# Kernel optimization log

Hardware: AMD Instinct MI355X
Metric: run time of the kernel (lower is better)

Reference implementation:

```python
import jax, jax.numpy as jnp
import numpy as np

D_MODEL = 1024
N_HEADS = 16
D_K = D_MODEL // N_HEADS
D_FF = 4 * D_MODEL
LN_EPS = 1e-5


def _layer_norm(x, gamma, beta):
    mu = jnp.mean(x, axis=-1, keepdims=True)
    var = jnp.mean(jnp.square(x - mu), axis=-1, keepdims=True)
    return (x - mu) * jax.lax.rsqrt(var + LN_EPS) * gamma + beta


def setup_inputs() -> dict:
    key = jax.random.key(0)
    ks = jax.random.split(key, 16)
    s = 1.0 / np.sqrt(D_MODEL)
    sf = 1.0 / np.sqrt(D_FF)
    return {
        "x": jax.random.normal(ks[0], (4, 2048, D_MODEL), dtype=jnp.float32),
        "ln1_g": jnp.ones((D_MODEL,), jnp.float32),
        "ln1_b": jnp.zeros((D_MODEL,), jnp.float32),
        "ln2_g": jnp.ones((D_MODEL,), jnp.float32),
        "ln2_b": jnp.zeros((D_MODEL,), jnp.float32),
        "Wq": jax.random.uniform(ks[1], (D_MODEL, D_MODEL), jnp.float32, -s, s),
        "bq": jax.random.uniform(ks[2], (D_MODEL,), jnp.float32, -s, s),
        "Wk": jax.random.uniform(ks[3], (D_MODEL, D_MODEL), jnp.float32, -s, s),
        "bk": jax.random.uniform(ks[4], (D_MODEL,), jnp.float32, -s, s),
        "Wv": jax.random.uniform(ks[5], (D_MODEL, D_MODEL), jnp.float32, -s, s),
        "bv": jax.random.uniform(ks[6], (D_MODEL,), jnp.float32, -s, s),
        "Wo": jax.random.uniform(ks[7], (D_MODEL, D_MODEL), jnp.float32, -s, s),
        "bo": jax.random.uniform(ks[8], (D_MODEL,), jnp.float32, -s, s),
        "W1": jax.random.uniform(ks[9], (D_MODEL, D_FF), jnp.float32, -s, s),
        "b1": jax.random.uniform(ks[10], (D_FF,), jnp.float32, -s, s),
        "W2": jax.random.uniform(ks[11], (D_FF, D_MODEL), jnp.float32, -sf, sf),
        "b2": jax.random.uniform(ks[12], (D_MODEL,), jnp.float32, -sf, sf),
    }


def reference(x, ln1_g, ln1_b, ln2_g, ln2_b, Wq, bq, Wk, bk, Wv, bv, Wo, bo, W1, b1, W2, b2):
    B, S, _ = x.shape
    # --- pre-LN multi-head attention (dropout=0, mask=None) ---
    xn = _layer_norm(x, ln1_g, ln1_b)                      # [B,S,D]
    q = (xn @ Wq + bq).reshape(B, S, N_HEADS, D_K)          # [B,S,H,Dk]
    k = (xn @ Wk + bk).reshape(B, S, N_HEADS, D_K)
    v = (xn @ Wv + bv).reshape(B, S, N_HEADS, D_K)
    scores = jnp.einsum("bqhd,bkhd->bhqk", q, k) / np.sqrt(D_K)  # [B,H,S,S]
    attn = jax.nn.softmax(scores, axis=-1)
    ctx = jnp.einsum("bhqk,bkhd->bqhd", attn, v).reshape(B, S, D_MODEL)
    x = x + (ctx @ Wo + bo)
    # --- pre-LN FFN ---
    xn = _layer_norm(x, ln2_g, ln2_b)
    h = jax.nn.relu(xn @ W1 + b1)                           # [B,S,4D]
    x = x + (h @ W2 + b2)
    return x
```

## Files before the change

kernel.cpp:

```cpp
#include <hip/hip_runtime.h>
#include <cstdint>

typedef unsigned short u16;
typedef unsigned int u32;
typedef __bf16 bf16x8 __attribute__((ext_vector_type(8)));
typedef float f32x4 __attribute__((ext_vector_type(4)));
typedef u16 u16x8 __attribute__((ext_vector_type(8)));
typedef u32 u32x2 __attribute__((ext_vector_type(2)));

#define GLOBAL_AS __attribute__((address_space(1)))
#define LDS_AS __attribute__((address_space(3)))

__device__ __forceinline__ u16 f2b(float f) {
  u32 u = __builtin_bit_cast(u32, f);
  u += 0x7fffu + ((u >> 16) & 1u);
  return (u16)(u >> 16);
}

__global__ void transpose_cvt(const float* __restrict__ in, u16* __restrict__ out,
                              int K, int N) {
  __shared__ float tile[32][33];
  const int tx = threadIdx.x, ty = threadIdx.y;
  const int n0 = blockIdx.x * 32, k0 = blockIdx.y * 32;
#pragma unroll
  for (int i = 0; i < 4; i++)
    tile[ty + i * 8][tx] = in[(size_t)(k0 + ty + i * 8) * N + n0 + tx];
  __syncthreads();
#pragma unroll
  for (int i = 0; i < 4; i++)
    out[(size_t)(n0 + ty + i * 8) * K + k0 + tx] = f2b(tile[tx][ty + i * 8]);
}

__global__ __launch_bounds__(256) void ln_fwd(const float* __restrict__ x,
                                              const float* __restrict__ gamma,
                                              const float* __restrict__ beta,
                                              u16* __restrict__ out) {
  const int wid = threadIdx.x >> 6, lane = threadIdx.x & 63;
  const size_t row = (size_t)blockIdx.x * 4 + wid;
  const float* xr = x + row * 1024;
  float4 v[4];
  float s = 0.f, s2 = 0.f;
#pragma unroll
  for (int i = 0; i < 4; i++) {
    v[i] = *(const float4*)(xr + i * 256 + lane * 4);
    s += v[i].x + v[i].y + v[i].z + v[i].w;
    s2 += v[i].x * v[i].x + v[i].y * v[i].y + v[i].z * v[i].z + v[i].w * v[i].w;
  }
#pragma unroll
  for (int m = 1; m < 64; m <<= 1) {
    s += __shfl_xor(s, m);
    s2 += __shfl_xor(s2, m);
  }
  const float mu = s * (1.f / 1024.f);
  const float var = s2 * (1.f / 1024.f) - mu * mu;
  const float rs = rsqrtf(var + 1e-5f);
  u16* orow = out + row * 1024;
#pragma unroll
  for (int i = 0; i < 4; i++) {
    float4 gv = *(const float4*)(gamma + i * 256 + lane * 4);
    float4 bv = *(const float4*)(beta + i * 256 + lane * 4);
    float y0 = (v[i].x - mu) * rs * gv.x + bv.x;
    float y1 = (v[i].y - mu) * rs * gv.y + bv.y;
    float y2 = (v[i].z - mu) * rs * gv.z + bv.z;
    float y3 = (v[i].w - mu) * rs * gv.w + bv.w;
    uint2 pk;
    pk.x = (u32)f2b(y0) | ((u32)f2b(y1) << 16);
    pk.y = (u32)f2b(y2) | ((u32)f2b(y3) << 16);
    *(uint2*)(orow + i * 256 + lane * 4) = pk;
  }
}

template <int MODE>
__global__ __launch_bounds__(256) void gemm_bt(
    const u16* __restrict__ A, const u16* __restrict__ BT,
    const float* __restrict__ b0, const float* __restrict__ b1,
    const float* __restrict__ b2, const float* __restrict__ res,
    void* __restrict__ outp, int M, int N, int K) {
  __shared__ __align__(16) u16 Alds[128 * 64];
  __shared__ __align__(16) u16 Blds[128 * 64];
  const int tid = threadIdx.x;
  const int wid = tid >> 6, lane = tid & 63;
  const int wm = wid >> 1, wn = wid & 1;
  const int g = lane >> 4, l15 = lane & 15;
  const int bm = blockIdx.y * 128, bn = blockIdx.x * 128;

  f32x4 acc[4][4] = {};

  const int srow = wid * 32 + (lane >> 3);
  const int scol = (lane & 7) * 8;
  const u16* Ag = A + (size_t)(bm + srow) * K + scol;
  const u16* Bg = BT + (size_t)(bn + srow) * K + scol;

  for (int k0 = 0; k0 < K; k0 += 64) {
    __syncthreads();
#pragma unroll
    for (int i = 0; i < 4; i++)
      __builtin_amdgcn_global_load_lds(
          (const GLOBAL_AS u32*)(Ag + (size_t)(i * 8) * K + k0),
          (LDS_AS u32*)&Alds[(wid * 32 + i * 8) * 64], 16, 0, 0);
#pragma unroll
    for (int i = 0; i < 4; i++)
      __builtin_amdgcn_global_load_lds(
          (const GLOBAL_AS u32*)(Bg + (size_t)(i * 8) * K + k0),
          (LDS_AS u32*)&Blds[(wid * 32 + i * 8) * 64], 16, 0, 0);
    __syncthreads();
#pragma unroll
    for (int ks = 0; ks < 2; ks++) {
      bf16x8 af[4], bfr[4];
#pragma unroll
      for (int mt = 0; mt < 4; mt++)
        af[mt] = *(const bf16x8*)&Alds[(wm * 64 + mt * 16 + l15) * 64 + ks * 32 + g * 8];
#pragma unroll
      for (int nt = 0; nt < 4; nt++)
        bfr[nt] = *(const bf16x8*)&Blds[(wn * 64 + nt * 16 + l15) * 64 + ks * 32 + g * 8];
#pragma unroll
      for (int mt = 0; mt < 4; mt++)
#pragma unroll
        for (int nt = 0; nt < 4; nt++)
          acc[mt][nt] = __builtin_amdgcn_mfma_f32_16x16x32_bf16(
              af[mt], bfr[nt], acc[mt][nt], 0, 0, 0);
    }
  }

  const float* bias = b0;
  float scale = 1.f;
  if (MODE == 0) {
    bias = (bn < 1024) ? b0 : (bn < 2048 ? b1 : b2);
    if (bn < 1024) scale = 0.18033688011112042f;
  }
#pragma unroll
  for (int mt = 0; mt < 4; mt++) {
#pragma unroll
    for (int nt = 0; nt < 4; nt++) {
      const int orow = bm + wm * 64 + mt * 16 + g * 4;
      const int ocol = bn + wn * 64 + nt * 16 + l15;
      const float bv = bias[MODE == 0 ? (ocol & 1023) : ocol];
#pragma unroll
      for (int r = 0; r < 4; r++) {
        const float v = acc[mt][nt][r] + bv;
        const size_t oi = (size_t)(orow + r) * N + ocol;
        if (MODE == 0)
          ((u16*)outp)[oi] = f2b(v * scale);
        else if (MODE == 1)
          ((u16*)outp)[oi] = f2b(v > 0.f ? v : 0.f);
        else
          ((float*)outp)[oi] = v + res[oi];
      }
    }
  }
}

__global__ __launch_bounds__(256) void attn_fwd(const u16* __restrict__ QKV,
                                                u16* __restrict__ ctx) {
  __shared__ __align__(16) u16 Klds[2][64 * 64];
  __shared__ __align__(16) u16 Vlds[2][64 * 64];
  const int tid = threadIdx.x;
  const int wid = tid >> 6, lane = tid & 63;
  const int g = lane >> 4, l15 = lane & 15;
  const int qt = blockIdx.x, h = blockIdx.y, b = blockIdx.z;

  const u16* Qbase = QKV + (size_t)(b * 2048 + qt * 64 + wid * 16) * 3072 + h * 64;
  bf16x8 qf[2];
#pragma unroll
  for (int ks = 0; ks < 2; ks++)
    qf[ks] = *(const bf16x8*)(Qbase + (size_t)l15 * 3072 + ks * 32 + g * 8);

  const u16* Kg = QKV + (size_t)(b * 2048) * 3072 + 1024 + h * 64;
  const u16* Vg = QKV + (size_t)(b * 2048) * 3072 + 2048 + h * 64;

  int kvK[2], colK[2], kvV[2], d0V[2];
#pragma unroll
  for (int i = 0; i < 2; i++) {
    const int p = tid + 256 * i;
    kvK[i] = p >> 3;
    colK[i] = ((p & 7) ^ (kvK[i] & 7)) << 3;
    kvV[i] = ((p >> 5) << 2) | ((p >> 1) & 3);
    d0V[i] = (((p >> 3) & 3) << 4) | ((p & 1) << 3);
  }

#define STAGE(bufidx, tt)                                                          \
  do {                                                                             \
    const size_t roff = (size_t)(tt) * 64 * 3072;                                  \
    _Pragma("unroll") for (int i = 0; i < 2; i++) {                                \
      __builtin_amdgcn_global_load_lds(                                            \
          (const GLOBAL_AS u32*)(Kg + roff + (size_t)kvK[i] * 3072 + colK[i]),     \
          (LDS_AS u32*)&Klds[bufidx][(i * 256 + wid * 64) * 8], 16, 0, 0);         \
      __builtin_amdgcn_global_load_lds(                                            \
          (const GLOBAL_AS u32*)(Vg + roff + (size_t)kvV[i] * 3072 + d0V[i]),      \
          (LDS_AS u32*)&Vlds[bufidx][(i * 256 + wid * 64) * 8], 16, 0, 0);         \
    }                                                                              \
  } while (0)

#define TRISSUE(dst, dtc)                                                          \
  do {                                                                             \
    _Pragma("unroll") for (int nt = 0; nt < 4; nt++) {                             \
      const u32 a_ = vb + (u32)((((nt * 4 + g) * 4 + (dtc)) << 7) + (l15 << 1));   \
      asm volatile("ds_read_b64_tr_b16 %0, %1" : "=v"(dst[nt]) : "v"(a_)           \
                   : "memory");                                                    \
    }                                                                              \
  } while (0)

  float mrun = -3.0e38f, lrun = 0.f;
  f32x4 cacc[4] = {};

  STAGE(0, 0);
  int cur = 0;
  for (int t = 0; t < 32; t++) {
    __syncthreads();
    if (t < 31) STAGE(cur ^ 1, t + 1);

    const u16* Kc = &Klds[cur][0];
    f32x4 s4[4] = {};
#pragma unroll
    for (int nt = 0; nt < 4; nt++) {
      const int kv = nt * 16 + l15;
      const int sw = kv & 7;
#pragma unroll
      for (int ks = 0; ks < 2; ks++) {
        bf16x8 kf = *(const bf16x8*)&Kc[kv * 64 + (((ks * 4 + g) ^ sw) << 3)];
        s4[nt] = __builtin_amdgcn_mfma_f32_16x16x32_bf16(kf, qf[ks], s4[nt], 0, 0, 0);
      }
    }

    float pm = s4[0][0];
#pragma unroll
    for (int nt = 0; nt < 4; nt++)
#pragma unroll
      for (int r = 0; r < 4; r++) pm = fmaxf(pm, s4[nt][r]);
    pm = fmaxf(pm, __shfl_xor(pm, 16));
    pm = fmaxf(pm, __shfl_xor(pm, 32));
    const float mn = fmaxf(mrun, pm);
    const float alpha = exp2f(mrun - mn);
    mrun = mn;

    float psum = 0.f;
    u32 w[4][2];
#pragma unroll
    for (int nt = 0; nt < 4; nt++) {
      const float p0 = exp2f(s4[nt][0] - mn);
      const float p1 = exp2f(s4[nt][1] - mn);
      const float p2 = exp2f(s4[nt][2] - mn);
      const float p3 = exp2f(s4[nt][3] - mn);
      psum += (p0 + p1) + (p2 + p3);
      asm("v_cvt_pk_bf16_f32 %0, %1, %2" : "=v"(w[nt][0]) : "v"(p0), "v"(p1));
      asm("v_cvt_pk_bf16_f32 %0, %1, %2" : "=v"(w[nt][1]) : "v"(p2), "v"(p3));
    }
    psum += __shfl_xor(psum, 16);
    psum += __shfl_xor(psum, 32);
    lrun = lrun * alpha + psum;
#pragma unroll
    for (int dt = 0; dt < 4; dt++) cacc[dt] *= alpha;

    const u32 vb = (u32)(uintptr_t)(const LDS_AS u16*)&Vlds[cur][0];
    u32x2 vf[2][4];
    TRISSUE(vf[0], 0);
#pragma unroll
    for (int dt = 0; dt < 4; dt++) {
      if (dt < 3) TRISSUE(vf[(dt + 1) & 1], dt + 1);
      if (dt < 3)
        asm volatile("s_waitcnt lgkmcnt(4)" ::: "memory");
      else
        asm volatile("s_waitcnt lgkmcnt(0)" ::: "memory");
      __builtin_amdgcn_sched_barrier(0);
#pragma unroll
      for (int nt = 0; nt < 4; nt++) {
        const u32x2 pf = {w[nt][0], w[nt][1]};
        asm volatile("v_mfma_f32_16x16x16_bf16 %0, %1, %2, %0"
                     : "+v"(cacc[dt])
                     : "v"(vf[dt & 1][nt]), "v"(pf));
      }
    }
    cur ^= 1;
  }
#undef STAGE
#undef TRISSUE

  asm volatile("s_nop 7" :::);
  asm volatile("s_nop 7" :::);

  const float inv = 1.f / lrun;
  u16* op = ctx + (size_t)(b * 2048 + qt * 64 + wid * 16 + l15) * 1024 + h * 64 + g * 4;
#pragma unroll
  for (int dt = 0; dt < 4; dt++) {
    u32 lo, hi;
    const float c0 = cacc[dt][0] * inv, c1 = cacc[dt][1] * inv;
    const float c2 = cacc[dt][2] * inv, c3 = cacc[dt][3] * inv;
    asm("v_cvt_pk_bf16_f32 %0, %1, %2" : "=v"(lo) : "v"(c0), "v"(c1));
    asm("v_cvt_pk_bf16_f32 %0, %1, %2" : "=v"(hi) : "v"(c2), "v"(c3));
    *(u32x2*)(op + dt * 16) = (u32x2){lo, hi};
  }
}

extern "C" void kernel_launch(void* const* d_in, const int* in_sizes, int n_in,
                              void* d_out, int out_size, void* d_ws, size_t ws_size,
                              hipStream_t stream) {
  const float* x = (const float*)d_in[0];
  const float* ln1g = (const float*)d_in[1];
  const float* ln1b = (const float*)d_in[2];
  const float* ln2g = (const float*)d_in[3];
  const float* ln2b = (const float*)d_in[4];
  const float* Wq = (const float*)d_in[5];
  const float* bq = (const float*)d_in[6];
  const float* Wk = (const float*)d_in[7];
  const float* bk = (const float*)d_in[8];
  const float* Wv = (const float*)d_in[9];
  const float* bv = (const float*)d_in[10];
  const float* Wo = (const float*)d_in[11];
  const float* bo = (const float*)d_in[12];
  const float* W1 = (const float*)d_in[13];
  const float* b1 = (const float*)d_in[14];
  const float* W2 = (const float*)d_in[15];
  const float* b2 = (const float*)d_in[16];

  char* ws = (char*)d_ws;
  u16* WqkvT = (u16*)(ws + 0);
  u16* WoT = (u16*)(ws + 6291456);
  u16* W1T = (u16*)(ws + 8388608);
  u16* W2T = (u16*)(ws + 16777216);
  u16* xn = (u16*)(ws + 25165824);
  float* x2 = (float*)(ws + 41943040);
  u16* ctx = (u16*)(ws + 75497472);
  u16* big = (u16*)(ws + 92274688);
  u16* QKVb = big;
  u16* hbuf = big;
  float* outF = (float*)d_out;

  const dim3 tb(32, 8);
  transpose_cvt<<<dim3(32, 32), tb, 0, stream>>>(Wq, WqkvT, 1024, 1024);
  transpose_cvt<<<dim3(32, 32), tb, 0, stream>>>(Wk, WqkvT + 1024 * 1024, 1024, 1024);
  transpose_cvt<<<dim3(32, 32), tb, 0, stream>>>(Wv, WqkvT + 2048 * 1024, 1024, 1024);
  transpose_cvt<<<dim3(32, 32), tb, 0, stream>>>(Wo, WoT, 1024, 1024);
  transpose_cvt<<<dim3(128, 32), tb, 0, stream>>>(W1, W1T, 1024, 4096);
  transpose_cvt<<<dim3(32, 128), tb, 0, stream>>>(W2, W2T, 4096, 1024);

  ln_fwd<<<dim3(2048), dim3(256), 0, stream>>>(x, ln1g, ln1b, xn);
  gemm_bt<0><<<dim3(24, 64), dim3(256), 0, stream>>>(xn, WqkvT, bq, bk, bv, nullptr,
                                                     (void*)QKVb, 8192, 3072, 1024);
  attn_fwd<<<dim3(32, 16, 4), dim3(256), 0, stream>>>(QKVb, ctx);
  gemm_bt<2><<<dim3(8, 64), dim3(256), 0, stream>>>(ctx, WoT, bo, nullptr, nullptr, x,
                                                    (void*)x2, 8192, 1024, 1024);
  ln_fwd<<<dim3(2048), dim3(256), 0, stream>>>(x2, ln2g, ln2b, xn);
  gemm_bt<1><<<dim3(32, 64), dim3(256), 0, stream>>>(xn, W1T, b1, nullptr, nullptr,
                                                     nullptr, (void*)hbuf, 8192, 4096, 1024);
  gemm_bt<2><<<dim3(8, 64), dim3(256), 0, stream>>>(hbuf, W2T, b2, nullptr, nullptr, x2,
                                                    (void*)outF, 8192, 1024, 4096);
}
```

Measured before the change: 618.6 us.

## Replace GEMM with 8-wave double-buffered kernel using swizzled LDS and XCD tile remap

```diff
diff --git a/kernel.cpp b/kernel.cpp
--- a/kernel.cpp
+++ b/kernel.cpp
@@ -70,74 +70,122 @@
   }
 }
 
-template <int MODE>
-__global__ __launch_bounds__(256) void gemm_bt(
+template <int MF, int MODE>
+__global__ __launch_bounds__(512, 2) void gemm8p(
     const u16* __restrict__ A, const u16* __restrict__ BT,
     const float* __restrict__ b0, const float* __restrict__ b1,
     const float* __restrict__ b2, const float* __restrict__ res,
-    void* __restrict__ outp, int M, int N, int K) {
-  __shared__ __align__(16) u16 Alds[128 * 64];
-  __shared__ __align__(16) u16 Blds[128 * 64];
+    void* __restrict__ outp, int M, int N, int K, int gridN) {
+  constexpr int BM = MF * 32;
+  constexpr int AL = BM / 64;
+  __shared__ __align__(16) u16 Albuf[2][BM * 64];
+  __shared__ __align__(16) u16 Blbuf[2][256 * 64];
+
   const int tid = threadIdx.x;
-  const int wid = tid >> 6, lane = tid & 63;
-  const int wm = wid >> 1, wn = wid & 1;
+  const int lane = tid & 63, wid = tid >> 6;
+  const int wr = wid >> 2, wc = wid & 3;
   const int g = lane >> 4, l15 = lane & 15;
-  const int bm = blockIdx.y * 128, bn = blockIdx.x * 128;
-
-  f32x4 acc[4][4] = {};
-
-  const int srow = wid * 32 + (lane >> 3);
-  const int scol = (lane & 7) * 8;
-  const u16* Ag = A + (size_t)(bm + srow) * K + scol;
-  const u16* Bg = BT + (size_t)(bn + srow) * K + scol;
-
-  for (int k0 = 0; k0 < K; k0 += 64) {
-    __syncthreads();
-#pragma unroll
-    for (int i = 0; i < 4; i++)
-      __builtin_amdgcn_global_load_lds(
-          (const GLOBAL_AS u32*)(Ag + (size_t)(i * 8) * K + k0),
-          (LDS_AS u32*)&Alds[(wid * 32 + i * 8) * 64], 16, 0, 0);
-#pragma unroll
-    for (int i = 0; i < 4; i++)
-      __builtin_amdgcn_global_load_lds(
-          (const GLOBAL_AS u32*)(Bg + (size_t)(i * 8) * K + k0),
-          (LDS_AS u32*)&Blds[(wid * 32 + i * 8) * 64], 16, 0, 0);
-    __syncthreads();
-#pragma unroll
-    for (int ks = 0; ks < 2; ks++) {
-      bf16x8 af[4], bfr[4];
-#pragma unroll
-      for (int mt = 0; mt < 4; mt++)
-        af[mt] = *(const bf16x8*)&Alds[(wm * 64 + mt * 16 + l15) * 64 + ks * 32 + g * 8];
+  const int l8r = lane >> 3, l8c = lane & 7;
+
+  const int nwg = gridDim.x;
+  const int bid = blockIdx.x;
+  const int tile = (bid & 7) * (nwg >> 3) + (bid >> 3);
+  const int tm = tile / gridN, tn = tile - tm * gridN;
+  const int bm = tm * BM, bn = tn * 256;
+
+  const int scol = 8 * (l8c ^ l8r);
+  const u16* Ab = A + (size_t)(bm + wid * (AL * 8) + l8r) * K + scol;
+  const u16* Bb = BT + (size_t)(bn + wid * 32 + l8r) * K + scol;
+
+#define STAGE(bb, k0)                                                            \
+  do {                                                                           \
+    _Pragma("unroll") for (int i = 0; i < AL; i++)                               \
+        __builtin_amdgcn_global_load_lds(                                        \
+            (const GLOBAL_AS u32*)(Ab + (size_t)i * 8 * K + (k0)),               \
+            (LDS_AS u32*)&Albuf[bb][(wid * AL + i) * 512], 16, 0, 0);            \
+    _Pragma("unroll") for (int i = 0; i < 4; i++)                                \
+        __builtin_amdgcn_global_load_lds(                                        \
+            (const GLOBAL_AS u32*)(Bb + (size_t)i * 8 * K + (k0)),               \
+            (LDS_AS u32*)&Blbuf[bb][(wid * 4 + i) * 512], 16, 0, 0);             \
+  } while (0)
+
+#define VMCNT_STEADY()                                                           \
+  do {                                                                           \
+    if constexpr (MF == 8)                                                       \
+      asm volatile("s_waitcnt vmcnt(8)" ::: "memory");                           \
+    else                                                                         \
+      asm volatile("s_waitcnt vmcnt(6)" ::: "memory");                           \
+  } while (0)
+
+  f32x4 acc[MF][4] = {};
+  const int NT = K >> 6;
+
+  const int arow0 = (wr * (MF * 16) + l15) * 64;
+  const int brow0 = (wc * 64 + l15) * 64;
+  const int csw[2] = {8 * ((0 * 4 + g) ^ (l15 & 7)), 8 * ((1 * 4 + g) ^ (l15 & 7))};
+
+  STAGE(0, 0);
+  STAGE(1, 64);
+  VMCNT_STEADY();
+  __builtin_amdgcn_sched_barrier(0);
+  __builtin_amdgcn_s_barrier();
+
+  for (int t = 0; t < NT; t++) {
+    const int b = t & 1;
+    const u16* Alb = &Albuf[b][0];
+    const u16* Blb = &Blbuf[b][0];
+#pragma unroll
+    for (int q = 0; q < 4; q++) {
+      const int mh = q & 1, ks = q >> 1;
+      bf16x8 af[MF / 2], bf[4];
+#pragma unroll
+      for (int i = 0; i < MF / 2; i++)
+        af[i] = *(const bf16x8*)&Alb[arow0 + (mh * (MF / 2) + i) * (16 * 64) + csw[ks]];
 #pragma unroll
       for (int nt = 0; nt < 4; nt++)
-        bfr[nt] = *(const bf16x8*)&Blds[(wn * 64 + nt * 16 + l15) * 64 + ks * 32 + g * 8];
-#pragma unroll
-      for (int mt = 0; mt < 4; mt++)
+        bf[nt] = *(const bf16x8*)&Blb[brow0 + nt * (16 * 64) + csw[ks]];
+      __builtin_amdgcn_s_setprio(1);
+#pragma unroll
+      for (int i = 0; i < MF / 2; i++)
 #pragma unroll
         for (int nt = 0; nt < 4; nt++)
-          acc[mt][nt] = __builtin_amdgcn_mfma_f32_16x16x32_bf16(
-              af[mt], bfr[nt], acc[mt][nt], 0, 0, 0);
-    }
-  }
-
-  const float* bias = b0;
-  float scale = 1.f;
-  if (MODE == 0) {
-    bias = (bn < 1024) ? b0 : (bn < 2048 ? b1 : b2);
-    if (bn < 1024) scale = 0.18033688011112042f;
-  }
-#pragma unroll
-  for (int mt = 0; mt < 4; mt++) {
+          acc[mh * (MF / 2) + i][nt] = __builtin_amdgcn_mfma_f32_16x16x32_bf16(
+              af[i], bf[nt], acc[mh * (MF / 2) + i][nt], 0, 0, 0);
+      __builtin_amdgcn_s_setprio(0);
+    }
+    if (t + 1 < NT) {
+      __builtin_amdgcn_s_barrier();
+      if (t + 2 < NT) {
+        STAGE(b, (t + 2) * 64);
+        VMCNT_STEADY();
+      } else {
+        asm volatile("s_waitcnt vmcnt(0)" ::: "memory");
+      }
+      __builtin_amdgcn_sched_barrier(0);
+      __builtin_amdgcn_s_barrier();
+    }
+  }
+#undef STAGE
+#undef VMCNT_STEADY
+
+  const int orow0 = bm + wr * (MF * 16);
+  const int ocol0 = bn + wc * 64;
+#pragma unroll
+  for (int mf = 0; mf < MF; mf++) {
 #pragma unroll
     for (int nt = 0; nt < 4; nt++) {
-      const int orow = bm + wm * 64 + mt * 16 + g * 4;
-      const int ocol = bn + wn * 64 + nt * 16 + l15;
-      const float bv = bias[MODE == 0 ? (ocol & 1023) : ocol];
+      const int orow = orow0 + mf * 16 + g * 4;
+      const int ocol = ocol0 + nt * 16 + l15;
+      float bv, scale = 1.f;
+      if (MODE == 0) {
+        bv = (ocol < 1024) ? b0[ocol] : (ocol < 2048 ? b1[ocol - 1024] : b2[ocol - 2048]);
+        if (ocol < 1024) scale = 0.18033688011112042f;
+      } else {
+        bv = b0[ocol];
+      }
 #pragma unroll
       for (int r = 0; r < 4; r++) {
-        const float v = acc[mt][nt][r] + bv;
+        const float v = acc[mf][nt][r] + bv;
         const size_t oi = (size_t)(orow + r) * N + ocol;
         if (MODE == 0)
           ((u16*)outp)[oi] = f2b(v * scale);
@@ -334,14 +382,14 @@
   transpose_cvt<<<dim3(32, 128), tb, 0, stream>>>(W2, W2T, 4096, 1024);
 
   ln_fwd<<<dim3(2048), dim3(256), 0, stream>>>(x, ln1g, ln1b, xn);
-  gemm_bt<0><<<dim3(24, 64), dim3(256), 0, stream>>>(xn, WqkvT, bq, bk, bv, nullptr,
-                                                     (void*)QKVb, 8192, 3072, 1024);
+  gemm8p<8, 0><<<dim3(384), dim3(512), 0, stream>>>(xn, WqkvT, bq, bk, bv, nullptr,
+                                                    (void*)QKVb, 8192, 3072, 1024, 12);
   attn_fwd<<<dim3(32, 16, 4), dim3(256), 0, stream>>>(QKVb, ctx);
-  gemm_bt<2><<<dim3(8, 64), dim3(256), 0, stream>>>(ctx, WoT, bo, nullptr, nullptr, x,
-                                                    (void*)x2, 8192, 1024, 1024);
+  gemm8p<4, 2><<<dim3(256), dim3(512), 0, stream>>>(ctx, WoT, bo, nullptr, nullptr, x,
+                                                    (void*)x2, 8192, 1024, 1024, 4);
   ln_fwd<<<dim3(2048), dim3(256), 0, stream>>>(x2, ln2g, ln2b, xn);
-  gemm_bt<1><<<dim3(32, 64), dim3(256), 0, stream>>>(xn, W1T, b1, nullptr, nullptr,
-                                                     nullptr, (void*)hbuf, 8192, 4096, 1024);
-  gemm_bt<2><<<dim3(8, 64), dim3(256), 0, stream>>>(hbuf, W2T, b2, nullptr, nullptr, x2,
-                                                    (void*)outF, 8192, 1024, 4096);
-}
+  gemm8p<8, 1><<<dim3(512), dim3(512), 0, stream>>>(xn, W1T, b1, nullptr, nullptr,
+                                                    nullptr, (void*)hbuf, 8192, 4096, 1024, 16);
+  gemm8p<4, 2><<<dim3(256), dim3(512), 0, stream>>>(hbuf, W2T, b2, nullptr, nullptr, x2,
+                                                    (void*)outF, 8192, 1024, 4096, 4);
+}
```

New measurement: 586.7 us. 5.2% less time.
